# Optimization experiments

Hardware: AMD Instinct MI355X
Metric: run time of the kernel (lower is better)

Reference implementation:

```python
import jax, jax.numpy as jnp
import numpy as np

B, P, CIN, PS = 8192, 9, 12, 64   # batch, patches, channels, patch_size
D_IN = CIN * PS                    # 768 flattened patch features
ENC_H, D = 512, 1024               # patch_encoder_hidden, embedding_dim
E, EXP_H, C = 8, 2048, 1000        # num_experts, expert hidden, num_classes
SYM, SYM_H = 6, 64                 # symbolic_dim, symbolic gating hidden


def setup_inputs() -> dict:
    key = jax.random.key(0)
    ks = jax.random.split(key, 16)
    g = lambda k, shape, fan: jax.random.normal(k, shape, jnp.float32) / np.sqrt(fan)
    return {
        "patches": jax.random.normal(ks[0], (B, P, CIN, PS), jnp.float32),
        "symbolic_features": jax.random.normal(ks[1], (B, SYM), jnp.float32),
        # patch encoder (2-layer MLP per patch)
        "enc_w1": g(ks[2], (D_IN, ENC_H), D_IN), "enc_b1": jnp.zeros((ENC_H,), jnp.float32),
        "enc_w2": g(ks[3], (ENC_H, D), ENC_H),   "enc_b2": jnp.zeros((D,), jnp.float32),
        # neural gating: Linear(D,D)-ReLU-Linear(D,E)
        "gn_w1": g(ks[4], (D, D), D), "gn_b1": jnp.zeros((D,), jnp.float32),
        "gn_w2": g(ks[5], (D, E), D), "gn_b2": jnp.zeros((E,), jnp.float32),
        # symbolic gating: Linear(SYM,64)-ReLU-Linear(64,E)
        "gs_w1": g(ks[6], (SYM, SYM_H), SYM),  "gs_b1": jnp.zeros((SYM_H,), jnp.float32),
        "gs_w2": g(ks[7], (SYM_H, E), SYM_H),  "gs_b2": jnp.zeros((E,), jnp.float32),
        # stacked experts: Linear(D,H)-ReLU-(Dropout=eval identity)-Linear(H,C)
        "ew1": g(ks[8], (E, D, EXP_H), D),      "eb1": jnp.zeros((E, EXP_H), jnp.float32),
        "ew2": g(ks[9], (E, EXP_H, C), EXP_H),  "eb2": jnp.zeros((E, C), jnp.float32),
    }


def reference(patches, symbolic_features, enc_w1, enc_b1, enc_w2, enc_b2,
              gn_w1, gn_b1, gn_w2, gn_b2, gs_w1, gs_b1, gs_w2, gs_b2,
              ew1, eb1, ew2, eb2):
    b = patches.shape[0]
    # patch encoder: (b, P, CIN*PS) -> (b, P, D)
    x = patches.reshape(b, P, D_IN)
    h = jax.nn.relu(jnp.einsum('bpf,fh->bph', x, enc_w1) + enc_b1)
    encoded = jnp.einsum('bph,hd->bpd', h, enc_w2) + enc_b2
    # mean aggregation over patches
    agg = encoded.mean(axis=1)  # (b, D)
    # symbolic gating: 0.5*neural + 0.5*symbolic logits, softmax
    neural = jax.nn.relu(agg @ gn_w1 + gn_b1) @ gn_w2 + gn_b2            # (b, E)
    symb = jax.nn.relu(symbolic_features @ gs_w1 + gs_b1) @ gs_w2 + gs_b2  # (b, E)
    gating_weights = jax.nn.softmax(0.5 * neural + 0.5 * symb, axis=1)
    # all experts densely (batched over expert axis)
    eh = jax.nn.relu(jnp.einsum('bd,edh->beh', agg, ew1) + eb1)          # (b, E, H)
    expert_logits = jnp.einsum('beh,ehc->bec', eh, ew2) + eb2            # (b, E, C)
    # gate-weighted sum
    logits = jnp.einsum('be,bec->bc', gating_weights, expert_logits)     # (b, C)
    return logits, gating_weights, expert_logits
```

## Files before the change

kernel.cpp:

```cpp
#include <hip/hip_runtime.h>
#include <hip/hip_bf16.h>

typedef __attribute__((ext_vector_type(8))) short s16x8;
typedef __attribute__((ext_vector_type(4))) float f32x4;

#define DEV __device__ __forceinline__

DEV short f2b(float f) {
  __hip_bfloat16 h = __float2bfloat16(f);
  short s; __builtin_memcpy(&s, &h, 2); return s;
}
DEV float b2f(short s) {
  __hip_bfloat16 h; __builtin_memcpy(&h, &s, 2); return __bfloat162float(h);
}

typedef __attribute__((address_space(1))) const void gvoid;
typedef __attribute__((address_space(3))) void lvoid;
DEV void gload_lds16(const void* g, void* l) {
  __builtin_amdgcn_global_load_lds((gvoid*)g, (lvoid*)l, 16, 0, 0);
}

static constexpr int kB = 8192, kP = 9, kDIN = 768, kENCH = 512, kD = 1024;
static constexpr int kE = 8, kH = 2048, kC = 1000;
static constexpr size_t OUT_GATE   = (size_t)kB * kC;
static constexpr size_t OUT_EL     = OUT_GATE + (size_t)kB * kE;

static constexpr size_t W1T  = 0;
static constexpr size_t W2T  = W1T  + 786432;
static constexpr size_t GW1T = W2T  + 1048576;
static constexpr size_t EW1T = GW1T + 2097152;
static constexpr size_t EW2T = EW1T + 33554432;
static constexpr size_t PBF  = EW2T + 32768000;
static constexpr size_t HBUF = PBF  + 113246208;
static constexpr size_t EH4  = HBUF + 75497472;
static constexpr size_t HMEAN = PBF;
static constexpr size_t AGG   = HMEAN + 8388608;
static constexpr size_t GH    = AGG   + 16777216;
static constexpr size_t NEU   = GH    + 16777216;
static constexpr size_t SYMB  = NEU   + 262144;

__global__ void cast_bf16_kernel(const float* __restrict__ in, short* __restrict__ out, size_t n8) {
  size_t i = (size_t)blockIdx.x * blockDim.x + threadIdx.x;
  if (i >= n8) return;
  float4 a = ((const float4*)in)[i * 2];
  float4 b = ((const float4*)in)[i * 2 + 1];
  s16x8 v;
  v[0] = f2b(a.x); v[1] = f2b(a.y); v[2] = f2b(a.z); v[3] = f2b(a.w);
  v[4] = f2b(b.x); v[5] = f2b(b.y); v[6] = f2b(b.z); v[7] = f2b(b.w);
  *(s16x8*)(out + i * 8) = v;
}

__global__ void transpose_cast_kernel(const float* __restrict__ in, short* __restrict__ out,
                                      int R, int C, size_t istride, size_t ostride) {
  __shared__ float tile[32][33];
  const float* W = in + istride * blockIdx.z;
  short* T = out + ostride * blockIdx.z;
  int tx = threadIdx.x, ty = threadIdx.y;
  int c0 = blockIdx.x * 32, r0 = blockIdx.y * 32;
  #pragma unroll
  for (int i = 0; i < 32; i += 8) {
    int r = r0 + ty + i, c = c0 + tx;
    if (r < R && c < C) tile[ty + i][tx] = W[(size_t)r * C + c];
  }
  __syncthreads();
  #pragma unroll
  for (int i = 0; i < 32; i += 8) {
    int rr = c0 + ty + i, cc = r0 + tx;
    if (rr < C && cc < R) T[(size_t)rr * R + cc] = f2b(tile[tx][ty + i]);
  }
}

#define BARR() __builtin_amdgcn_s_barrier()
#define VMW6() asm volatile("s_waitcnt vmcnt(6)" ::: "memory")
#define VMW4() asm volatile("s_waitcnt vmcnt(4)" ::: "memory")
#define VMW0() asm volatile("s_waitcnt vmcnt(0)" ::: "memory")

template<bool RELU, bool F32OUT, bool NTAIL>
__global__ __launch_bounds__(512, 2)
void gemm256_kernel(const short* __restrict__ A, const short* __restrict__ Bt,
                    const float* __restrict__ bias, void* __restrict__ Cout,
                    int M, int N, int K, int ldc,
                    long aZ, long bZ, long biasZ, long cZ) {
  __shared__ short Abuf[2][2][8192];
  __shared__ short Bbuf[2][2][8192];
  const int z = blockIdx.z;
  A += (size_t)z * aZ; Bt += (size_t)z * bZ; bias += (size_t)z * biasZ;

  const int XT = gridDim.x;
  int lid = blockIdx.y * XT + blockIdx.x;
  const int cpx = (XT * gridDim.y) >> 3;
  lid = (lid & 7) * cpx + (lid >> 3);
  const int bx = lid % XT, by = lid / XT;
  const int bM = by * 256, bN = bx * 256;

  const int t = threadIdx.x, lane = t & 63, wid = t >> 6;
  const int wm = wid & 1, wn = wid >> 1;
  const int lr = lane & 15, kg = lane >> 4;
  const int nkt = K >> 6;

  const int srB = t >> 3;
  const int sx = (t & 7) ^ (srB & 7);
  const int ldsoff = wid * 512;

  int ar0 = bM + srB, ar1 = bM + 64 + srB, ar2 = bM + 128 + srB, ar3 = bM + 192 + srB;
  int br0 = bN + srB, br1 = bN + 64 + srB, br2 = bN + 128 + srB, br3 = bN + 192 + srB;
  if (NTAIL) {
    if (br0 >= N) br0 = N - 1;
    if (br1 >= N) br1 = N - 1;
    if (br2 >= N) br2 = N - 1;
    if (br3 >= N) br3 = N - 1;
  }
  const short* pA00 = A + (size_t)ar0 * K + sx * 8;
  const short* pA01 = A + (size_t)ar1 * K + sx * 8;
  const short* pA10 = A + (size_t)ar2 * K + sx * 8;
  const short* pA11 = A + (size_t)ar3 * K + sx * 8;
  const short* pB00 = Bt + (size_t)br0 * K + sx * 8;
  const short* pB01 = Bt + (size_t)br1 * K + sx * 8;
  const short* pB10 = Bt + (size_t)br2 * K + sx * 8;
  const short* pB11 = Bt + (size_t)br3 * K + sx * 8;

#define STAGE_A0(tile_) do { if ((tile_) < nkt) { int par_ = (tile_) & 1; \
    gload_lds16(pA00, &Abuf[par_][0][ldsoff]); \
    gload_lds16(pA01, &Abuf[par_][0][4096 + ldsoff]); \
    pA00 += 64; pA01 += 64; } } while (0)
#define STAGE_A1(tile_) do { if ((tile_) < nkt) { int par_ = (tile_) & 1; \
    gload_lds16(pA10, &Abuf[par_][1][ldsoff]); \
    gload_lds16(pA11, &Abuf[par_][1][4096 + ldsoff]); \
    pA10 += 64; pA11 += 64; } } while (0)
#define STAGE_B0(tile_) do { if ((tile_) < nkt) { int par_ = (tile_) & 1; \
    gload_lds16(pB00, &Bbuf[par_][0][ldsoff]); \
    gload_lds16(pB01, &Bbuf[par_][0][4096 + ldsoff]); \
    pB00 += 64; pB01 += 64; } } while (0)
#define STAGE_B1(tile_) do { if ((tile_) < nkt) { int par_ = (tile_) & 1; \
    gload_lds16(pB10, &Bbuf[par_][1][ldsoff]); \
    gload_lds16(pB11, &Bbuf[par_][1][4096 + ldsoff]); \
    pB10 += 64; pB11 += 64; } } while (0)

  const int aro = (wm * 64 + lr) * 64;
  const int bro = (wn * 32 + lr) * 64;
  const int so0 = (kg ^ (lr & 7)) * 8;
  const int so1 = ((4 + kg) ^ (lr & 7)) * 8;

  s16x8 a0[4][2], a1[4][2], b0[2][2], b1[2][2];
#define LDA0(par_) do { _Pragma("unroll") \
    for (int m_ = 0; m_ < 4; ++m_) { \
      a0[m_][0] = *(const s16x8*)&Abuf[par_][0][aro + m_ * 1024 + so0]; \
      a0[m_][1] = *(const s16x8*)&Abuf[par_][0][aro + m_ * 1024 + so1]; \
    } } while (0)
#define LDA1(par_) do { _Pragma("unroll") \
    for (int m_ = 0; m_ < 4; ++m_) { \
      a1[m_][0] = *(const s16x8*)&Abuf[par_][1][aro + m_ * 1024 + so0]; \
      a1[m_][1] = *(const s16x8*)&Abuf[par_][1][aro + m_ * 1024 + so1]; \
    } } while (0)
#define LDB0(par_) do { _Pragma("unroll") \
    for (int n_ = 0; n_ < 2; ++n_) { \
      b0[n_][0] = *(const s16x8*)&Bbuf[par_][0][bro + n_ * 1024 + so0]; \
      b0[n_][1] = *(const s16x8*)&Bbuf[par_][0][bro + n_ * 1024 + so1]; \
    } } while (0)
#define LDB1(par_) do { _Pragma("unroll") \
    for (int n_ = 0; n_ < 2; ++n_) { \
      b1[n_][0] = *(const s16x8*)&Bbuf[par_][1][bro + n_ * 1024 + so0]; \
      b1[n_][1] = *(const s16x8*)&Bbuf[par_][1][bro + n_ * 1024 + so1]; \
    } } while (0)

  f32x4 acc[2][2][4][2];
  #pragma unroll
  for (int a_ = 0; a_ < 2; ++a_)
    #pragma unroll
    for (int b_ = 0; b_ < 2; ++b_)
      #pragma unroll
      for (int m_ = 0; m_ < 4; ++m_)
        #pragma unroll
        for (int n_ = 0; n_ < 2; ++n_) acc[a_][b_][m_][n_] = (f32x4){0.f, 0.f, 0.f, 0.f};

#define MMAQ(mh, nh, AF, BF) do { \
    __builtin_amdgcn_s_setprio(1); \
    _Pragma("unroll") \
    for (int m_ = 0; m_ < 4; ++m_) \
      _Pragma("unroll") \
      for (int n_ = 0; n_ < 2; ++n_) { \
        acc[mh][nh][m_][n_] = __builtin_amdgcn_mfma_f32_16x16x32_bf16(AF[m_][0], BF[n_][0], acc[mh][nh][m_][n_], 0, 0, 0); \
        acc[mh][nh][m_][n_] = __builtin_amdgcn_mfma_f32_16x16x32_bf16(AF[m_][1], BF[n_][1], acc[mh][nh][m_][n_], 0, 0, 0); \
      } \
    __builtin_amdgcn_s_setprio(0); } while (0)

  STAGE_A0(0); STAGE_B0(0); STAGE_B1(0); STAGE_A1(0);
  VMW4();
  STAGE_A0(1); STAGE_B0(1); STAGE_B1(1);
  VMW6();
  BARR();

  for (int g = 0; g < nkt; ++g) {
    const int par = g & 1;
    LDA0(par); LDB0(par);
    STAGE_A1(g + 1);
    BARR();
    MMAQ(0, 0, a0, b0);
    BARR();
    LDB1(par);
    STAGE_A0(g + 2);
    BARR();
    MMAQ(0, 1, a0, b1);
    BARR();
    LDA1(par);
    STAGE_B0(g + 2);
    BARR();
    MMAQ(1, 1, a1, b1);
    BARR();
    STAGE_B1(g + 2);
    if (g == nkt - 2) { VMW0(); } else if (g < nkt - 2) { VMW6(); }
    BARR();
    MMAQ(1, 0, a1, b0);
    BARR();
  }

  #pragma unroll
  for (int nh = 0; nh < 2; ++nh)
    #pragma unroll
    for (int n_ = 0; n_ < 2; ++n_) {
      int col = bN + nh * 128 + wn * 32 + n_ * 16 + lr;
      if (NTAIL && col >= N) continue;
      float bv = bias[col];
      #pragma unroll
      for (int mh = 0; mh < 2; ++mh)
        #pragma unroll
        for (int m_ = 0; m_ < 4; ++m_) {
          int row0 = bM + mh * 128 + wm * 64 + m_ * 16 + kg * 4;
          #pragma unroll
          for (int r_ = 0; r_ < 4; ++r_) {
            float v = acc[mh][nh][m_][n_][r_] + bv;
            if (RELU) v = fmaxf(v, 0.f);
            size_t off = (size_t)(row0 + r_) * ldc + col;
            if (F32OUT) ((float*)Cout + (size_t)z * cZ)[off] = v;
            else        ((short*)Cout + (size_t)z * cZ)[off] = f2b(v);
          }
        }
    }
#undef STAGE_A0
#undef STAGE_A1
#undef STAGE_B0
#undef STAGE_B1
#undef LDA0
#undef LDA1
#undef LDB0
#undef LDB1
#undef MMAQ
}

template<bool RELU, bool F32OUT>
__global__ __launch_bounds__(256, 2)
void gemm_bt_kernel(const short* __restrict__ A, const short* __restrict__ Bt,
                    const float* __restrict__ bias, void* __restrict__ Cout,
                    int M, int N, int K, int ldc) {
  __shared__ short As[128 * 32];
  __shared__ short Bs[128 * 32];
  const int t = threadIdx.x;
  const int lane = t & 63, wid = t >> 6;
  const int wr = wid >> 1, wc = wid & 1;
  const int lr = lane & 15, lk8 = (lane >> 4) * 8;
  const int arow0 = blockIdx.y * 128;
  const int bcol0 = blockIdx.x * 128;

  f32x4 acc[4][4];
  #pragma unroll
  for (int m = 0; m < 4; ++m)
    #pragma unroll
    for (int n = 0; n < 4; ++n) acc[m][n] = (f32x4){0.f, 0.f, 0.f, 0.f};

  const int srow = t >> 2, sseg = (t & 3) * 8;
  const short* ga0 = A + (size_t)(arow0 + srow) * K + sseg;
  const short* ga1 = ga0 + (size_t)64 * K;
  int br0 = bcol0 + srow;      if (br0 >= N) br0 = N - 1;
  int br1 = bcol0 + srow + 64; if (br1 >= N) br1 = N - 1;
  const short* gb0 = Bt + (size_t)br0 * K + sseg;
  const short* gb1 = Bt + (size_t)br1 * K + sseg;
  short* lA0 = As + wid * 512;
  short* lA1 = As + 2048 + wid * 512;
  short* lB0 = Bs + wid * 512;
  short* lB1 = Bs + 2048 + wid * 512;

  for (int k0 = 0; k0 < K; k0 += 32) {
    __syncthreads();
    gload_lds16(ga0, lA0);
    gload_lds16(ga1, lA1);
    gload_lds16(gb0, lB0);
    gload_lds16(gb1, lB1);
    ga0 += 32; ga1 += 32; gb0 += 32; gb1 += 32;
    __syncthreads();
    s16x8 af[4], bfr[4];
    #pragma unroll
    for (int m = 0; m < 4; ++m) af[m] = *(const s16x8*)&As[(wr * 64 + m * 16 + lr) * 32 + lk8];
    #pragma unroll
    for (int n = 0; n < 4; ++n) bfr[n] = *(const s16x8*)&Bs[(wc * 64 + n * 16 + lr) * 32 + lk8];
    #pragma unroll
    for (int m = 0; m < 4; ++m)
      #pragma unroll
      for (int n = 0; n < 4; ++n)
        acc[m][n] = __builtin_amdgcn_mfma_f32_16x16x32_bf16(af[m], bfr[n], acc[m][n], 0, 0, 0);
  }

  #pragma unroll
  for (int n = 0; n < 4; ++n) {
    int col = bcol0 + wc * 64 + n * 16 + lr;
    if (col >= N) continue;
    float bv = bias[col];
    #pragma unroll
    for (int m = 0; m < 4; ++m) {
      int row0 = arow0 + wr * 64 + m * 16 + (lane >> 4) * 4;
      #pragma unroll
      for (int r = 0; r < 4; ++r) {
        float v = acc[m][n][r] + bv;
        if (RELU) v = fmaxf(v, 0.f);
        size_t off = (size_t)(row0 + r) * ldc + col;
        if (F32OUT) ((float*)Cout)[off] = v;
        else        ((short*)Cout)[off] = f2b(v);
      }
    }
  }
}

__global__ void mean9_kernel(const short* __restrict__ h, short* __restrict__ hm) {
  size_t i = (size_t)blockIdx.x * blockDim.x + threadIdx.x;
  if (i >= (size_t)kB * kENCH / 8) return;
  size_t b = i >> 6; int d8 = (int)(i & 63);
  const short* base = h + b * kP * kENCH + d8 * 8;
  float s[8] = {0, 0, 0, 0, 0, 0, 0, 0};
  #pragma unroll
  for (int p = 0; p < kP; ++p) {
    s16x8 v = *(const s16x8*)(base + p * kENCH);
    #pragma unroll
    for (int j = 0; j < 8; ++j) s[j] += b2f(v[j]);
  }
  s16x8 o;
  #pragma unroll
  for (int j = 0; j < 8; ++j) o[j] = f2b(s[j] * (1.f / 9.f));
  *(s16x8*)(hm + i * 8) = o;
}

__global__ __launch_bounds__(256)
void gating_neural_kernel(const short* __restrict__ gh, const float* __restrict__ w2,
                          const float* __restrict__ b2, float* __restrict__ neural) {
  int wid = threadIdx.x >> 6, lane = threadIdx.x & 63;
  int row = blockIdx.x * 4 + wid;
  float acc[8] = {0,0,0,0,0,0,0,0};
  const short* grow = gh + (size_t)row * kD;
  for (int k = lane; k < kD; k += 64) {
    float x = b2f(grow[k]);
    const float* w = w2 + (size_t)k * 8;
    #pragma unroll
    for (int c = 0; c < 8; ++c) acc[c] += x * w[c];
  }
  #pragma unroll
  for (int c = 0; c < 8; ++c)
    #pragma unroll
    for (int off = 32; off >= 1; off >>= 1) acc[c] += __shfl_xor(acc[c], off);
  if (lane == 0) {
    #pragma unroll
    for (int c = 0; c < 8; ++c) neural[(size_t)row * 8 + c] = acc[c] + b2[c];
  }
}

__global__ __launch_bounds__(256)
void gating_symb_kernel(const float* __restrict__ sym, const float* __restrict__ w1,
                        const float* __restrict__ b1, const float* __restrict__ w2,
                        const float* __restrict__ b2, float* __restrict__ symb) {
  int wid = threadIdx.x >> 6, lane = threadIdx.x & 63;
  int row = blockIdx.x * 4 + wid;
  float s0 = sym[(size_t)row * 6 + 0], s1 = sym[(size_t)row * 6 + 1], s2 = sym[(size_t)row * 6 + 2];
  float s3 = sym[(size_t)row * 6 + 3], s4 = sym[(size_t)row * 6 + 4], s5 = sym[(size_t)row * 6 + 5];
  float hh = b1[lane];
  hh += s0 * w1[0 * 64 + lane] + s1 * w1[1 * 64 + lane] + s2 * w1[2 * 64 + lane];
  hh += s3 * w1[3 * 64 + lane] + s4 * w1[4 * 64 + lane] + s5 * w1[5 * 64 + lane];
  hh = fmaxf(hh, 0.f);
  float acc[8];
  #pragma unroll
  for (int c = 0; c < 8; ++c) acc[c] = hh * w2[lane * 8 + c];
  #pragma unroll
  for (int c = 0; c < 8; ++c)
    #pragma unroll
    for (int off = 32; off >= 1; off >>= 1) acc[c] += __shfl_xor(acc[c], off);
  if (lane == 0) {
    #pragma unroll
    for (int c = 0; c < 8; ++c) symb[(size_t)row * 8 + c] = acc[c] + b2[c];
  }
}

__global__ void gating_softmax_kernel(const float* __restrict__ neural, const float* __restrict__ symb,
                                      float* __restrict__ gate_out) {
  int row = blockIdx.x * blockDim.x + threadIdx.x;
  if (row >= kB) return;
  float g[8], m = -1e30f;
  #pragma unroll
  for (int c = 0; c < 8; ++c) {
    g[c] = 0.5f * (neural[(size_t)row * 8 + c] + symb[(size_t)row * 8 + c]);
    m = fmaxf(m, g[c]);
  }
  float sum = 0.f;
  #pragma unroll
  for (int c = 0; c < 8; ++c) { g[c] = expf(g[c] - m); sum += g[c]; }
  float inv = 1.f / sum;
  #pragma unroll
  for (int c = 0; c < 8; ++c) gate_out[(size_t)row * 8 + c] = g[c] * inv;
}

__global__ __launch_bounds__(256)
void combine_kernel(float* __restrict__ out) {
  int b = blockIdx.y;
  int c = blockIdx.x * 256 + threadIdx.x;
  __shared__ float g[8];
  if (threadIdx.x < 8) g[threadIdx.x] = out[OUT_GATE + (size_t)b * 8 + threadIdx.x];
  __syncthreads();
  if (c < kC) {
    const float* el = out + OUT_EL + (size_t)b * (kE * kC) + c;
    float a = 0.f;
    #pragma unroll
    for (int e = 0; e < 8; ++e) a += g[e] * el[e * kC];
    out[(size_t)b * kC + c] = a;
  }
}

static void launch_gemm128(bool relu, bool f32out, const short* A, const short* Bt, const float* bias,
                           void* C, int M, int N, int K, int ldc, hipStream_t s) {
  dim3 g((N + 127) / 128, M / 128), b(256);
  if (relu && !f32out)       gemm_bt_kernel<true,  false><<<g, b, 0, s>>>(A, Bt, bias, C, M, N, K, ldc);
  else if (!relu && !f32out) gemm_bt_kernel<false, false><<<g, b, 0, s>>>(A, Bt, bias, C, M, N, K, ldc);
  else if (relu && f32out)   gemm_bt_kernel<true,  true ><<<g, b, 0, s>>>(A, Bt, bias, C, M, N, K, ldc);
  else                       gemm_bt_kernel<false, true ><<<g, b, 0, s>>>(A, Bt, bias, C, M, N, K, ldc);
}

extern "C" void kernel_launch(void* const* d_in, const int* in_sizes, int n_in,
                              void* d_out, int out_size, void* d_ws, size_t ws_size,
                              hipStream_t stream) {
  const float* patches = (const float*)d_in[0];
  const float* symf    = (const float*)d_in[1];
  const float* enc_w1  = (const float*)d_in[2];
  const float* enc_b1  = (const float*)d_in[3];
  const float* enc_w2  = (const float*)d_in[4];
  const float* enc_b2  = (const float*)d_in[5];
  const float* gn_w1   = (const float*)d_in[6];
  const float* gn_b1   = (const float*)d_in[7];
  const float* gn_w2   = (const float*)d_in[8];
  const float* gn_b2   = (const float*)d_in[9];
  const float* gs_w1   = (const float*)d_in[10];
  const float* gs_b1   = (const float*)d_in[11];
  const float* gs_w2   = (const float*)d_in[12];
  const float* gs_b2   = (const float*)d_in[13];
  const float* ew1     = (const float*)d_in[14];
  const float* eb1     = (const float*)d_in[15];
  const float* ew2     = (const float*)d_in[16];
  const float* eb2     = (const float*)d_in[17];
  char* ws = (char*)d_ws;
  float* out = (float*)d_out;
  dim3 tb(32, 8);

  {
    size_t n8 = (size_t)kB * kP * kDIN / 8;
    cast_bf16_kernel<<<(unsigned)((n8 + 255) / 256), 256, 0, stream>>>(patches, (short*)(ws + PBF), n8);
  }
  transpose_cast_kernel<<<dim3(16, 24, 1), tb, 0, stream>>>(enc_w1, (short*)(ws + W1T),  kDIN,  kENCH, 0, 0);
  transpose_cast_kernel<<<dim3(32, 16, 1), tb, 0, stream>>>(enc_w2, (short*)(ws + W2T),  kENCH, kD,    0, 0);
  transpose_cast_kernel<<<dim3(32, 32, 1), tb, 0, stream>>>(gn_w1,  (short*)(ws + GW1T), kD,    kD,    0, 0);
  transpose_cast_kernel<<<dim3(64, 32, 8), tb, 0, stream>>>(ew1,    (short*)(ws + EW1T), kD,    kH,
                                                            (size_t)kD * kH, (size_t)kD * kH);
  transpose_cast_kernel<<<dim3(32, 64, 8), tb, 0, stream>>>(ew2,    (short*)(ws + EW2T), kH,    kC,
                                                            (size_t)kH * kC, (size_t)kH * kC);
  gemm256_kernel<true, false, false><<<dim3(2, 288, 1), 512, 0, stream>>>(
      (short*)(ws + PBF), (short*)(ws + W1T), enc_b1, ws + HBUF,
      kB * kP, kENCH, kDIN, kENCH, 0, 0, 0, 0);
  mean9_kernel<<<(kB * kENCH / 8) / 256, 256, 0, stream>>>((short*)(ws + HBUF), (short*)(ws + HMEAN));
  launch_gemm128(false, false, (short*)(ws + HMEAN), (short*)(ws + W2T), enc_b2,
                 ws + AGG, kB, kD, kENCH, kD, stream);
  launch_gemm128(true, false, (short*)(ws + AGG), (short*)(ws + GW1T), gn_b1,
                 ws + GH, kB, kD, kD, kD, stream);
  gating_neural_kernel<<<kB / 4, 256, 0, stream>>>((short*)(ws + GH), gn_w2, gn_b2, (float*)(ws + NEU));
  gating_symb_kernel<<<kB / 4, 256, 0, stream>>>(symf, gs_w1, gs_b1, gs_w2, gs_b2, (float*)(ws + SYMB));
  gating_softmax_kernel<<<kB / 256, 256, 0, stream>>>((float*)(ws + NEU), (float*)(ws + SYMB), out + OUT_GATE);
  for (int h = 0; h < 2; ++h) {
    int e0 = h * 4;
    gemm256_kernel<true, false, false><<<dim3(8, 32, 4), 512, 0, stream>>>(
        (short*)(ws + AGG), (short*)(ws + EW1T) + (size_t)e0 * kH * kD, eb1 + (size_t)e0 * kH,
        ws + EH4, kB, kH, kD, kH,
        0, (long)kH * kD, kH, (long)kB * kH);
    gemm256_kernel<false, true, true><<<dim3(4, 32, 4), 512, 0, stream>>>(
        (short*)(ws + EH4), (short*)(ws + EW2T) + (size_t)e0 * kC * kH, eb2 + (size_t)e0 * kC,
        out + OUT_EL + (size_t)e0 * kC, kB, kC, kH, kE * kC,
        (long)kB * kH, (long)kC * kH, kC, kC);
  }
  combine_kernel<<<dim3(4, kB), 256, 0, stream>>>(out);
}
```

Before: 1.016 ms.

## Fuse gate combine into expert GEMM epilogue, drop barriers, reuse 256 GEMM

```diff
diff --git a/kernel.cpp b/kernel.cpp
--- a/kernel.cpp
+++ b/kernel.cpp
@@ -50,6 +50,11 @@
   *(s16x8*)(out + i * 8) = v;
 }
 
+__global__ void zero_logits_kernel(float4* __restrict__ p, size_t n4) {
+  size_t i = (size_t)blockIdx.x * blockDim.x + threadIdx.x;
+  if (i < n4) p[i] = (float4){0.f, 0.f, 0.f, 0.f};
+}
+
 __global__ void transpose_cast_kernel(const float* __restrict__ in, short* __restrict__ out,
                                       int R, int C, size_t istride, size_t ostride) {
   __shared__ float tile[32][33];
@@ -75,12 +80,13 @@
 #define VMW4() asm volatile("s_waitcnt vmcnt(4)" ::: "memory")
 #define VMW0() asm volatile("s_waitcnt vmcnt(0)" ::: "memory")
 
-template<bool RELU, bool F32OUT, bool NTAIL>
+template<bool RELU, bool F32OUT, bool NTAIL, bool FUSEL>
 __global__ __launch_bounds__(512, 2)
 void gemm256_kernel(const short* __restrict__ A, const short* __restrict__ Bt,
                     const float* __restrict__ bias, void* __restrict__ Cout,
                     int M, int N, int K, int ldc,
-                    long aZ, long bZ, long biasZ, long cZ) {
+                    long aZ, long bZ, long biasZ, long cZ,
+                    const float* __restrict__ gate, float* __restrict__ logits, int eBase) {
   __shared__ short Abuf[2][2][8192];
   __shared__ short Bbuf[2][2][8192];
   const int z = blockIdx.z;
@@ -102,7 +108,6 @@
   const int sx = (t & 7) ^ (srB & 7);
   const int ldsoff = wid * 512;
 
-  int ar0 = bM + srB, ar1 = bM + 64 + srB, ar2 = bM + 128 + srB, ar3 = bM + 192 + srB;
   int br0 = bN + srB, br1 = bN + 64 + srB, br2 = bN + 128 + srB, br3 = bN + 192 + srB;
   if (NTAIL) {
     if (br0 >= N) br0 = N - 1;
@@ -110,10 +115,10 @@
     if (br2 >= N) br2 = N - 1;
     if (br3 >= N) br3 = N - 1;
   }
-  const short* pA00 = A + (size_t)ar0 * K + sx * 8;
-  const short* pA01 = A + (size_t)ar1 * K + sx * 8;
-  const short* pA10 = A + (size_t)ar2 * K + sx * 8;
-  const short* pA11 = A + (size_t)ar3 * K + sx * 8;
+  const short* pA00 = A + (size_t)(bM + srB) * K + sx * 8;
+  const short* pA01 = A + (size_t)(bM + 64 + srB) * K + sx * 8;
+  const short* pA10 = A + (size_t)(bM + 128 + srB) * K + sx * 8;
+  const short* pA11 = A + (size_t)(bM + 192 + srB) * K + sx * 8;
   const short* pB00 = Bt + (size_t)br0 * K + sx * 8;
   const short* pB01 = Bt + (size_t)br1 * K + sx * 8;
   const short* pB10 = Bt + (size_t)br2 * K + sx * 8;
@@ -194,23 +199,19 @@
     const int par = g & 1;
     LDA0(par); LDB0(par);
     STAGE_A1(g + 1);
-    BARR();
     MMAQ(0, 0, a0, b0);
     BARR();
     LDB1(par);
     STAGE_A0(g + 2);
-    BARR();
     MMAQ(0, 1, a0, b1);
     BARR();
     LDA1(par);
     STAGE_B0(g + 2);
-    BARR();
     MMAQ(1, 1, a1, b1);
     BARR();
     STAGE_B1(g + 2);
+    MMAQ(1, 0, a1, b0);
     if (g == nkt - 2) { VMW0(); } else if (g < nkt - 2) { VMW6(); }
-    BARR();
-    MMAQ(1, 0, a1, b0);
     BARR();
   }
 
@@ -233,6 +234,10 @@
             size_t off = (size_t)(row0 + r_) * ldc + col;
             if (F32OUT) ((float*)Cout + (size_t)z * cZ)[off] = v;
             else        ((short*)Cout + (size_t)z * cZ)[off] = f2b(v);
+            if (FUSEL) {
+              float gv = gate[(size_t)(row0 + r_) * kE + eBase + z];
+              atomicAdd(logits + (size_t)(row0 + r_) * kC + col, gv * v);
+            }
           }
         }
     }
@@ -245,78 +250,6 @@
 #undef LDB0
 #undef LDB1
 #undef MMAQ
-}
-
-template<bool RELU, bool F32OUT>
-__global__ __launch_bounds__(256, 2)
-void gemm_bt_kernel(const short* __restrict__ A, const short* __restrict__ Bt,
-                    const float* __restrict__ bias, void* __restrict__ Cout,
-                    int M, int N, int K, int ldc) {
-  __shared__ short As[128 * 32];
-  __shared__ short Bs[128 * 32];
-  const int t = threadIdx.x;
-  const int lane = t & 63, wid = t >> 6;
-  const int wr = wid >> 1, wc = wid & 1;
-  const int lr = lane & 15, lk8 = (lane >> 4) * 8;
-  const int arow0 = blockIdx.y * 128;
-  const int bcol0 = blockIdx.x * 128;
-
-  f32x4 acc[4][4];
-  #pragma unroll
-  for (int m = 0; m < 4; ++m)
-    #pragma unroll
-    for (int n = 0; n < 4; ++n) acc[m][n] = (f32x4){0.f, 0.f, 0.f, 0.f};
-
-  const int srow = t >> 2, sseg = (t & 3) * 8;
-  const short* ga0 = A + (size_t)(arow0 + srow) * K + sseg;
-  const short* ga1 = ga0 + (size_t)64 * K;
-  int br0 = bcol0 + srow;      if (br0 >= N) br0 = N - 1;
-  int br1 = bcol0 + srow + 64; if (br1 >= N) br1 = N - 1;
-  const short* gb0 = Bt + (size_t)br0 * K + sseg;
-  const short* gb1 = Bt + (size_t)br1 * K + sseg;
-  short* lA0 = As + wid * 512;
-  short* lA1 = As + 2048 + wid * 512;
-  short* lB0 = Bs + wid * 512;
-  short* lB1 = Bs + 2048 + wid * 512;
-
-  for (int k0 = 0; k0 < K; k0 += 32) {
-    __syncthreads();
-    gload_lds16(ga0, lA0);
-    gload_lds16(ga1, lA1);
-    gload_lds16(gb0, lB0);
-    gload_lds16(gb1, lB1);
-    ga0 += 32; ga1 += 32; gb0 += 32; gb1 += 32;
-    __syncthreads();
-    s16x8 af[4], bfr[4];
-    #pragma unroll
-    for (int m = 0; m < 4; ++m) af[m] = *(const s16x8*)&As[(wr * 64 + m * 16 + lr) * 32 + lk8];
-    #pragma unroll
-    for (int n = 0; n < 4; ++n) bfr[n] = *(const s16x8*)&Bs[(wc * 64 + n * 16 + lr) * 32 + lk8];
-    #pragma unroll
-    for (int m = 0; m < 4; ++m)
-      #pragma unroll
-      for (int n = 0; n < 4; ++n)
-        acc[m][n] = __builtin_amdgcn_mfma_f32_16x16x32_bf16(af[m], bfr[n], acc[m][n], 0, 0, 0);
-  }
-
-  #pragma unroll
-  for (int n = 0; n < 4; ++n) {
-    int col = bcol0 + wc * 64 + n * 16 + lr;
-    if (col >= N) continue;
-    float bv = bias[col];
-    #pragma unroll
-    for (int m = 0; m < 4; ++m) {
-      int row0 = arow0 + wr * 64 + m * 16 + (lane >> 4) * 4;
-      #pragma unroll
-      for (int r = 0; r < 4; ++r) {
-        float v = acc[m][n][r] + bv;
-        if (RELU) v = fmaxf(v, 0.f);
-        size_t off = (size_t)(row0 + r) * ldc + col;
-        if (F32OUT) ((float*)Cout)[off] = v;
-        else        ((short*)Cout)[off] = f2b(v);
-      }
-    }
-  }
 }
 
 __global__ void mean9_kernel(const short* __restrict__ h, short* __restrict__ hm) {
@@ -401,31 +334,6 @@
   float inv = 1.f / sum;
   #pragma unroll
   for (int c = 0; c < 8; ++c) gate_out[(size_t)row * 8 + c] = g[c] * inv;
-}
-
-__global__ __launch_bounds__(256)
-void combine_kernel(float* __restrict__ out) {
-  int b = blockIdx.y;
-  int c = blockIdx.x * 256 + threadIdx.x;
-  __shared__ float g[8];
-  if (threadIdx.x < 8) g[threadIdx.x] = out[OUT_GATE + (size_t)b * 8 + threadIdx.x];
-  __syncthreads();
-  if (c < kC) {
-    const float* el = out + OUT_EL + (size_t)b * (kE * kC) + c;
-    float a = 0.f;
-    #pragma unroll
-    for (int e = 0; e < 8; ++e) a += g[e] * el[e * kC];
-    out[(size_t)b * kC + c] = a;
-  }
-}
-
-static void launch_gemm128(bool relu, bool f32out, const short* A, const short* Bt, const float* bias,
-                           void* C, int M, int N, int K, int ldc, hipStream_t s) {
-  dim3 g((N + 127) / 128, M / 128), b(256);
-  if (relu && !f32out)       gemm_bt_kernel<true,  false><<<g, b, 0, s>>>(A, Bt, bias, C, M, N, K, ldc);
-  else if (!relu && !f32out) gemm_bt_kernel<false, false><<<g, b, 0, s>>>(A, Bt, bias, C, M, N, K, ldc);
-  else if (relu && f32out)   gemm_bt_kernel<true,  true ><<<g, b, 0, s>>>(A, Bt, bias, C, M, N, K, ldc);
-  else                       gemm_bt_kernel<false, true ><<<g, b, 0, s>>>(A, Bt, bias, C, M, N, K, ldc);
 }
 
 extern "C" void kernel_launch(void* const* d_in, const int* in_sizes, int n_in,
@@ -464,27 +372,32 @@
                                                             (size_t)kD * kH, (size_t)kD * kH);
   transpose_cast_kernel<<<dim3(32, 64, 8), tb, 0, stream>>>(ew2,    (short*)(ws + EW2T), kH,    kC,
                                                             (size_t)kH * kC, (size_t)kH * kC);
-  gemm256_kernel<true, false, false><<<dim3(2, 288, 1), 512, 0, stream>>>(
+  gemm256_kernel<true, false, false, false><<<dim3(2, 288, 1), 512, 0, stream>>>(
       (short*)(ws + PBF), (short*)(ws + W1T), enc_b1, ws + HBUF,
-      kB * kP, kENCH, kDIN, kENCH, 0, 0, 0, 0);
+      kB * kP, kENCH, kDIN, kENCH, 0, 0, 0, 0, nullptr, nullptr, 0);
   mean9_kernel<<<(kB * kENCH / 8) / 256, 256, 0, stream>>>((short*)(ws + HBUF), (short*)(ws + HMEAN));
-  launch_gemm128(false, false, (short*)(ws + HMEAN), (short*)(ws + W2T), enc_b2,
-                 ws + AGG, kB, kD, kENCH, kD, stream);
-  launch_gemm128(true, false, (short*)(ws + AGG), (short*)(ws + GW1T), gn_b1,
-                 ws + GH, kB, kD, kD, kD, stream);
+  gemm256_kernel<false, false, false, false><<<dim3(4, 32, 1), 512, 0, stream>>>(
+      (short*)(ws + HMEAN), (short*)(ws + W2T), enc_b2, ws + AGG,
+      kB, kD, kENCH, kD, 0, 0, 0, 0, nullptr, nullptr, 0);
+  gemm256_kernel<true, false, false, false><<<dim3(4, 32, 1), 512, 0, stream>>>(
+      (short*)(ws + AGG), (short*)(ws + GW1T), gn_b1, ws + GH,
+      kB, kD, kD, kD, 0, 0, 0, 0, nullptr, nullptr, 0);
   gating_neural_kernel<<<kB / 4, 256, 0, stream>>>((short*)(ws + GH), gn_w2, gn_b2, (float*)(ws + NEU));
   gating_symb_kernel<<<kB / 4, 256, 0, stream>>>(symf, gs_w1, gs_b1, gs_w2, gs_b2, (float*)(ws + SYMB));
   gating_softmax_kernel<<<kB / 256, 256, 0, stream>>>((float*)(ws + NEU), (float*)(ws + SYMB), out + OUT_GATE);
+  {
+    size_t n4 = (size_t)kB * kC / 4;
+    zero_logits_kernel<<<(unsigned)((n4 + 255) / 256), 256, 0, stream>>>((float4*)out, n4);
+  }
   for (int h = 0; h < 2; ++h) {
     int e0 = h * 4;
-    gemm256_kernel<true, false, false><<<dim3(8, 32, 4), 512, 0, stream>>>(
+    gemm256_kernel<true, false, false, false><<<dim3(8, 32, 4), 512, 0, stream>>>(
         (short*)(ws + AGG), (short*)(ws + EW1T) + (size_t)e0 * kH * kD, eb1 + (size_t)e0 * kH,
         ws + EH4, kB, kH, kD, kH,
-        0, (long)kH * kD, kH, (long)kB * kH);
-    gemm256_kernel<false, true, true><<<dim3(4, 32, 4), 512, 0, stream>>>(
+        0, (long)kH * kD, kH, (long)kB * kH, nullptr, nullptr, 0);
+    gemm256_kernel<false, true, true, true><<<dim3(4, 32, 4), 512, 0, stream>>>(
         (short*)(ws + EH4), (short*)(ws + EW2T) + (size_t)e0 * kC * kH, eb2 + (size_t)e0 * kC,
         out + OUT_EL + (size_t)e0 * kC, kB, kC, kH, kE * kC,
-        (long)kB * kH, (long)kC * kH, kC, kC);
-  }
-  combine_kernel<<<dim3(4, kB), 256, 0, stream>>>(out);
-}
+        (long)kB * kH, (long)kC * kH, kC, kC, out + OUT_GATE, out, e0);
+  }
+}
```

Result: slower. 1.232 ms (+21.3%).
